# Performance work log

Hardware: AMD Instinct MI355X
Metric: run time of the kernel (lower is better)

Reference implementation:

```python
import jax, jax.numpy as jnp
import numpy as np

N_NODES = 100000
D = 128


def gcn_conv(x, W, b, src, dst, deg_inv_sqrt):
    # PyG GCNConv: linear transform, symmetric-normalized aggregation with self-loops, bias
    h = x @ W  # [N, D_out]
    norm = deg_inv_sqrt[src] * deg_inv_sqrt[dst]  # [E_tot]
    msgs = h[src] * norm[:, None]  # gather + scale  [E_tot, D_out]
    out = jax.ops.segment_sum(msgs, dst, num_segments=x.shape[0])  # scatter-add to targets
    return out + b


def _prep_edges(edge_index, n_nodes):
    # add self-loops (weight 1) and compute deg^{-1/2} over targets (flow source_to_target)
    loops = jnp.arange(n_nodes, dtype=edge_index.dtype)
    src = jnp.concatenate([edge_index[0], loops])
    dst = jnp.concatenate([edge_index[1], loops])
    deg = jax.ops.segment_sum(jnp.ones_like(dst, dtype=jnp.float32), dst, num_segments=n_nodes)
    deg_inv_sqrt = jnp.where(deg > 0, jax.lax.rsqrt(jnp.maximum(deg, 1.0)), 0.0)
    return src, dst, deg_inv_sqrt


def setup_inputs() -> dict:
    key = jax.random.key(0)
    ks = jax.random.split(key, 8)
    node_fts = jax.random.normal(ks[0], (N_NODES, D), dtype=jnp.float32)
    edge_index = jax.random.randint(ks[1], (2, 1600000), 0, N_NODES, dtype=jnp.int64)
    scale = 1.0 / np.sqrt(D)
    W1 = jax.random.uniform(ks[2], (D, D), jnp.float32, -scale, scale)
    b1 = jnp.zeros((D,), jnp.float32)
    W2 = jax.random.uniform(ks[3], (D, D), jnp.float32, -scale, scale)
    b2 = jnp.zeros((D,), jnp.float32)
    W3 = jax.random.uniform(ks[4], (D, D), jnp.float32, -scale, scale)
    b3 = jnp.zeros((D,), jnp.float32)
    return {"node_fts": node_fts, "edge_index": edge_index,
            "W1": W1, "b1": b1, "W2": W2, "b2": b2, "W3": W3, "b3": b3}


def reference(node_fts, edge_index, W1, b1, W2, b2, W3, b3):
    n = node_fts.shape[0]
    src, dst, dinv = _prep_edges(edge_index, n)
    x = jax.nn.relu(gcn_conv(node_fts, W1, b1, src, dst, dinv))
    x = jax.nn.relu(gcn_conv(x, W2, b2, src, dst, dinv))
    x = jax.nn.relu(gcn_conv(x, W3, b3, src, dst, dinv))
    return x
```

## Files before the change

kernel.cpp:

```cpp
#include <hip/hip_runtime.h>

#define NN 100000
#define EE 1600000
#define D 128
#define STRIDE 64
#define NPART 8
#define PSZ (NN / NPART)
#define NI4 (EE / 4)

typedef __attribute__((ext_vector_type(8))) short bf16x8;
typedef __attribute__((ext_vector_type(4))) float f32x4;

__device__ inline unsigned int f2bf2(float a, float b) {
    unsigned int ua = __float_as_uint(a);
    unsigned int ub = __float_as_uint(b);
    ua = (ua + 0x7fffu + ((ua >> 16) & 1u)) >> 16;
    ub = (ub + 0x7fffu + ((ub >> 16) & 1u)) >> 16;
    return ua | (ub << 16);
}
__device__ inline unsigned short f2bf(float a) {
    unsigned int u = __float_as_uint(a);
    return (unsigned short)((u + 0x7fffu + ((u >> 16) & 1u)) >> 16);
}
__device__ inline float2 bf2f2(unsigned int u) {
    return make_float2(__uint_as_float(u << 16), __uint_as_float(u & 0xffff0000u));
}


__global__ void init_kernel(int* __restrict__ cursor, unsigned int* __restrict__ hb) {
    int i = blockIdx.x * blockDim.x + threadIdx.x;
    if (i < NN) cursor[i] = 0;
    if (i < 64) hb[(size_t)NN * 64 + i] = 0;
}

__global__ __launch_bounds__(256) void scatter_part_kernel(const int4* __restrict__ src4,
                                                           const int4* __restrict__ dst4,
                                                           int* __restrict__ cursor,
                                                           int* __restrict__ csr) {
    const int p = blockIdx.x & (NPART - 1);
    const int bp = blockIdx.x >> 3;
    const int lo = p * PSZ, hi = lo + PSZ;
    for (int j = bp * 256 + threadIdx.x; j < NI4; j += 256 * 256) {
        int4 d4 = dst4[j];
        bool m0 = (d4.x >= lo && d4.x < hi);
        bool m1 = (d4.y >= lo && d4.y < hi);
        bool m2 = (d4.z >= lo && d4.z < hi);
        bool m3 = (d4.w >= lo && d4.w < hi);
        if (!(m0 | m1 | m2 | m3)) continue;
        int4 s4 = src4[j];
        if (m0) csr[d4.x * STRIDE + atomicAdd(&cursor[d4.x], 1)] = s4.x;
        if (m1) csr[d4.y * STRIDE + atomicAdd(&cursor[d4.y], 1)] = s4.y;
        if (m2) csr[d4.z * STRIDE + atomicAdd(&cursor[d4.z], 1)] = s4.z;
        if (m3) csr[d4.w * STRIDE + atomicAdd(&cursor[d4.w], 1)] = s4.w;
    }
}

__global__ void dinv_pad_kernel(const int* __restrict__ cursor, float* __restrict__ dinv,
                                int* __restrict__ csr) {
    int i = blockIdx.x * blockDim.x + threadIdx.x;
    if (i < NN) {
        int c = cursor[i];
        dinv[i] = rsqrtf(1.0f + (float)c);
        int e = i * STRIDE + c;
        const int end = i * STRIDE + ((c + 7) & ~7);
        for (; e < end; ++e) csr[e] = NN;
    }
}

__global__ void wt_build3_kernel(const float* __restrict__ W1, const float* __restrict__ W2,
                                 const float* __restrict__ W3, unsigned short* __restrict__ wt1,
                                 unsigned short* __restrict__ wt2, unsigned short* __restrict__ wt3) {
    const int which = blockIdx.x >> 6;
    const float* W = which == 0 ? W1 : (which == 1 ? W2 : W3);
    unsigned short* wt = which == 0 ? wt1 : (which == 1 ? wt2 : wt3);
    int i = (blockIdx.x & 63) * 256 + threadIdx.x;
    int n = i >> 7, k = i & 127;
    wt[n * 128 + k] = f2bf(W[k * 128 + n]);
}


template <bool F32IN>
__global__ __launch_bounds__(256) void gemm_mfma_kernel(const void* __restrict__ xin,
                                                        const unsigned short* __restrict__ wt,
                                                        const float* __restrict__ dinv,
                                                        unsigned int* __restrict__ hb) {
    const int wave = blockIdx.x * 4 + (threadIdx.x >> 6);
    const int m0 = wave * 16;
    if (m0 >= NN) return;
    const int lane = threadIdx.x & 63;
    const int r = lane & 15;
    const int q = lane >> 4;
    const unsigned short* wrow = wt + (size_t)r * 128 + q * 8;
    f32x4 acc[8] = {};
#pragma unroll
    for (int kc = 0; kc < 4; ++kc) {
        bf16x8 xf;
        if (F32IN) {
            const float* xrow = (const float*)xin + (size_t)(m0 + r) * 128 + q * 8 + kc * 32;
            float4 a = *(const float4*)xrow;
            float4 b = *(const float4*)(xrow + 4);
            unsigned short tmp[8] = {f2bf(a.x), f2bf(a.y), f2bf(a.z), f2bf(a.w),
                                     f2bf(b.x), f2bf(b.y), f2bf(b.z), f2bf(b.w)};
            xf = *(const bf16x8*)tmp;
        } else {
            const unsigned short* xrow =
                (const unsigned short*)xin + (size_t)(m0 + r) * 128 + q * 8 + kc * 32;
            xf = *(const bf16x8*)xrow;
        }
#pragma unroll
        for (int nt = 0; nt < 8; ++nt) {
            bf16x8 wf = *(const bf16x8*)(wrow + (size_t)nt * 16 * 128 + kc * 32);
            acc[nt] = __builtin_amdgcn_mfma_f32_16x16x32_bf16(wf, xf, acc[nt], 0, 0, 0);
        }
    }
    const float dvr = dinv[m0 + r];
    unsigned int* hrow = hb + (size_t)(m0 + r) * 64;
#pragma unroll
    for (int nt = 0; nt < 8; ++nt) {
        int n = nt * 16 + q * 4;
        *(uint2*)(hrow + (n >> 1)) =
            make_uint2(f2bf2(acc[nt][0] * dvr, acc[nt][1] * dvr),
                       f2bf2(acc[nt][2] * dvr, acc[nt][3] * dvr));
    }
}


template <bool BF16OUT>
__global__ __launch_bounds__(256) void aggregate_kernel(const unsigned int* __restrict__ hb,
                                                        const int* __restrict__ csr,
                                                        const int* __restrict__ cursor,
                                                        const float* __restrict__ dinv,
                                                        const float2* __restrict__ bias2,
                                                        void* __restrict__ outp) {
    const int d = blockIdx.x * 4 + (threadIdx.x >> 6);
    const int j = threadIdx.x & 63;
    const int nb = (cursor[d] + 7) >> 3;
    const int base = d * STRIDE;
    float2 acc = bf2f2(hb[(size_t)d * 64 + j]);
    for (int b = 0; b < nb; ++b) {
        const int e = base + b * 8;
        int4 c0 = *(const int4*)(csr + e);
        int4 c1 = *(const int4*)(csr + e + 4);
        unsigned int v0 = hb[(size_t)c0.x * 64 + j];
        unsigned int v1 = hb[(size_t)c0.y * 64 + j];
        unsigned int v2 = hb[(size_t)c0.z * 64 + j];
        unsigned int v3 = hb[(size_t)c0.w * 64 + j];
        unsigned int v4 = hb[(size_t)c1.x * 64 + j];
        unsigned int v5 = hb[(size_t)c1.y * 64 + j];
        unsigned int v6 = hb[(size_t)c1.z * 64 + j];
        unsigned int v7 = hb[(size_t)c1.w * 64 + j];
        float2 f0 = bf2f2(v0), f1 = bf2f2(v1), f2 = bf2f2(v2), f3 = bf2f2(v3);
        float2 f4 = bf2f2(v4), f5 = bf2f2(v5), f6 = bf2f2(v6), f7 = bf2f2(v7);
        acc.x += f0.x + f1.x + f2.x + f3.x + f4.x + f5.x + f6.x + f7.x;
        acc.y += f0.y + f1.y + f2.y + f3.y + f4.y + f5.y + f6.y + f7.y;
    }
    const float dv = dinv[d];
    float2 bb = bias2[j];
    float ox = fmaxf(dv * acc.x + bb.x, 0.0f);
    float oy = fmaxf(dv * acc.y + bb.y, 0.0f);
    if (BF16OUT) {
        ((unsigned int*)outp)[(size_t)d * 64 + j] = f2bf2(ox, oy);
    } else {
        ((float2*)outp)[(size_t)d * 64 + j] = make_float2(ox, oy);
    }
}


extern "C" void kernel_launch(void* const* d_in, const int* in_sizes, int n_in,
                              void* d_out, int out_size, void* d_ws, size_t ws_size,
                              hipStream_t stream) {
    const float* x0 = (const float*)d_in[0];
    const int* ei = (const int*)d_in[1];
    const float* W1 = (const float*)d_in[2];
    const float* b1 = (const float*)d_in[3];
    const float* W2 = (const float*)d_in[4];
    const float* b2 = (const float*)d_in[5];
    const float* W3 = (const float*)d_in[6];
    const float* b3 = (const float*)d_in[7];
    float* out = (float*)d_out;

    char* ws = (char*)d_ws;
    size_t off = 0;
    auto alloc = [&](size_t bytes) -> void* {
        off = (off + 511) & ~(size_t)511;
        void* p = ws + off;
        off += bytes;
        return p;
    };
    unsigned int* hb  = (unsigned int*)alloc(((size_t)NN + 1) * 64 * 4);
    int*   csr    = (int*)  alloc((size_t)NN * STRIDE * sizeof(int));
    int*   cursor = (int*)  alloc((size_t)NN * sizeof(int));
    float* dinv   = (float*)alloc((size_t)NN * sizeof(float));
    unsigned short* wt1 = (unsigned short*)alloc(128 * 128 * 2);
    unsigned short* wt2 = (unsigned short*)alloc(128 * 128 * 2);
    unsigned short* wt3 = (unsigned short*)alloc(128 * 128 * 2);

    unsigned int* xact = (unsigned int*)d_out;

    const int4* src4 = (const int4*)ei;
    const int4* dst4 = (const int4*)(ei + EE);

    init_kernel<<<(NN + 255) / 256, 256, 0, stream>>>(cursor, hb);
    scatter_part_kernel<<<2048, 256, 0, stream>>>(src4, dst4, cursor, csr);
    dinv_pad_kernel<<<(NN + 255) / 256, 256, 0, stream>>>(cursor, dinv, csr);
    wt_build3_kernel<<<192, 256, 0, stream>>>(W1, W2, W3, wt1, wt2, wt3);

    const int gemmBlocks = (NN / 16 + 3) / 4;

    gemm_mfma_kernel<true><<<gemmBlocks, 256, 0, stream>>>((const void*)x0, wt1, dinv, hb);
    aggregate_kernel<true><<<NN / 4, 256, 0, stream>>>(hb, csr, cursor, dinv,
                                                       (const float2*)b1, (void*)xact);
    gemm_mfma_kernel<false><<<gemmBlocks, 256, 0, stream>>>((const void*)xact, wt2, dinv, hb);
    aggregate_kernel<true><<<NN / 4, 256, 0, stream>>>(hb, csr, cursor, dinv,
                                                       (const float2*)b2, (void*)xact);
    gemm_mfma_kernel<false><<<gemmBlocks, 256, 0, stream>>>((const void*)xact, wt3, dinv, hb);
    aggregate_kernel<false><<<NN / 4, 256, 0, stream>>>(hb, csr, cursor, dinv,
                                                        (const float2*)b3, (void*)out);
}
```

Before: 475.6 us.

## Bin edges by destination partition before CSR scatter and unroll aggregation by 16

Adds a binning pass that groups edges into eight destination-range buckets through shared-memory staging, so the CSR scatter reads each partition's edges once instead of every partition block scanning the full edge list. The scatter then walks its bucket in two sub-ranges to keep cursor atomics localized. The aggregation loop now gathers 16 neighbors per iteration with a tree reduction, raising memory-level parallelism. The bucket capacity assumes roughly uniform destinations and adds an extra workspace buffer plus a kernel launch.

```diff
diff --git a/kernel.cpp b/kernel.cpp
--- a/kernel.cpp
+++ b/kernel.cpp
@@ -6,7 +6,8 @@
 #define STRIDE 64
 #define NPART 8
 #define PSZ (NN / NPART)
-#define NI4 (EE / 4)
+#define BCAP 204800
+#define BINCAP 512
 
 typedef __attribute__((ext_vector_type(8))) short bf16x8;
 typedef __attribute__((ext_vector_type(4))) float f32x4;
@@ -27,31 +28,68 @@
 }
 
 
-__global__ void init_kernel(int* __restrict__ cursor, unsigned int* __restrict__ hb) {
+__global__ void init_kernel(int* __restrict__ cursor, int* __restrict__ gcur,
+                            unsigned int* __restrict__ hb) {
     int i = blockIdx.x * blockDim.x + threadIdx.x;
     if (i < NN) cursor[i] = 0;
+    if (i < NPART) gcur[i] = 0;
     if (i < 64) hb[(size_t)NN * 64 + i] = 0;
 }
 
-__global__ __launch_bounds__(256) void scatter_part_kernel(const int4* __restrict__ src4,
-                                                           const int4* __restrict__ dst4,
-                                                           int* __restrict__ cursor,
-                                                           int* __restrict__ csr) {
+__global__ __launch_bounds__(256) void bin_kernel(const int* __restrict__ src,
+                                                  const int* __restrict__ dst,
+                                                  int* __restrict__ gcur,
+                                                  uint2* __restrict__ buckets) {
+    __shared__ uint2 bins[NPART][BINCAP];
+    __shared__ int bcnt[NPART];
+    __shared__ int gbase[NPART];
+    if (threadIdx.x < NPART) bcnt[threadIdx.x] = 0;
+    __syncthreads();
+    const int per = (EE + gridDim.x - 1) / gridDim.x;
+    const int lo = blockIdx.x * per;
+    const int hi = min(lo + per, EE);
+    for (int i = lo + threadIdx.x; i < hi; i += 256) {
+        int s = src[i], d = dst[i];
+        int b = d / PSZ;
+        int pos = atomicAdd(&bcnt[b], 1);
+        if (pos < BINCAP) {
+            bins[b][pos] = make_uint2((unsigned)s, (unsigned)d);
+        } else {
+            int gp = atomicAdd(&gcur[b], 1);
+            buckets[(size_t)b * BCAP + gp] = make_uint2((unsigned)s, (unsigned)d);
+        }
+    }
+    __syncthreads();
+    if (threadIdx.x < NPART) {
+        int c = min(bcnt[threadIdx.x], BINCAP);
+        gbase[threadIdx.x] = atomicAdd(&gcur[threadIdx.x], c);
+        bcnt[threadIdx.x] = c;
+    }
+    __syncthreads();
+    for (int b = 0; b < NPART; ++b) {
+        const int c = bcnt[b];
+        uint2* outp = buckets + (size_t)b * BCAP + gbase[b];
+        for (int i = threadIdx.x; i < c; i += 256) outp[i] = bins[b][i];
+    }
+}
+
+__global__ __launch_bounds__(256) void scatter2_kernel(const uint2* __restrict__ buckets,
+                                                       const int* __restrict__ gcur,
+                                                       int* __restrict__ cursor,
+                                                       int* __restrict__ csr) {
     const int p = blockIdx.x & (NPART - 1);
     const int bp = blockIdx.x >> 3;
-    const int lo = p * PSZ, hi = lo + PSZ;
-    for (int j = bp * 256 + threadIdx.x; j < NI4; j += 256 * 256) {
-        int4 d4 = dst4[j];
-        bool m0 = (d4.x >= lo && d4.x < hi);
-        bool m1 = (d4.y >= lo && d4.y < hi);
-        bool m2 = (d4.z >= lo && d4.z < hi);
-        bool m3 = (d4.w >= lo && d4.w < hi);
-        if (!(m0 | m1 | m2 | m3)) continue;
-        int4 s4 = src4[j];
-        if (m0) csr[d4.x * STRIDE + atomicAdd(&cursor[d4.x], 1)] = s4.x;
-        if (m1) csr[d4.y * STRIDE + atomicAdd(&cursor[d4.y], 1)] = s4.y;
-        if (m2) csr[d4.z * STRIDE + atomicAdd(&cursor[d4.z], 1)] = s4.z;
-        if (m3) csr[d4.w * STRIDE + atomicAdd(&cursor[d4.w], 1)] = s4.w;
+    const int cnt = gcur[p];
+    const uint2* bk = buckets + (size_t)p * BCAP;
+    const int mid = p * PSZ + PSZ / 2;
+#pragma unroll
+    for (int sub = 0; sub < 2; ++sub) {
+        for (int i = bp * 256 + threadIdx.x; i < cnt; i += 256 * 256) {
+            uint2 e = bk[i];
+            int d = (int)e.y;
+            bool in = (sub == 0) ? (d < mid) : (d >= mid);
+            if (in) csr[d * STRIDE + atomicAdd(&cursor[d], 1)] = (int)e.x;
+        }
     }
 }
 
@@ -134,11 +172,41 @@
                                                         void* __restrict__ outp) {
     const int d = blockIdx.x * 4 + (threadIdx.x >> 6);
     const int j = threadIdx.x & 63;
-    const int nb = (cursor[d] + 7) >> 3;
     const int base = d * STRIDE;
+    int e = base;
+    const int end = base + ((cursor[d] + 7) & ~7);
     float2 acc = bf2f2(hb[(size_t)d * 64 + j]);
-    for (int b = 0; b < nb; ++b) {
-        const int e = base + b * 8;
+    for (; e + 16 <= end; e += 16) {
+        int4 c0 = *(const int4*)(csr + e);
+        int4 c1 = *(const int4*)(csr + e + 4);
+        int4 c2 = *(const int4*)(csr + e + 8);
+        int4 c3 = *(const int4*)(csr + e + 12);
+        unsigned int v0 = hb[(size_t)c0.x * 64 + j];
+        unsigned int v1 = hb[(size_t)c0.y * 64 + j];
+        unsigned int v2 = hb[(size_t)c0.z * 64 + j];
+        unsigned int v3 = hb[(size_t)c0.w * 64 + j];
+        unsigned int v4 = hb[(size_t)c1.x * 64 + j];
+        unsigned int v5 = hb[(size_t)c1.y * 64 + j];
+        unsigned int v6 = hb[(size_t)c1.z * 64 + j];
+        unsigned int v7 = hb[(size_t)c1.w * 64 + j];
+        unsigned int v8 = hb[(size_t)c2.x * 64 + j];
+        unsigned int v9 = hb[(size_t)c2.y * 64 + j];
+        unsigned int va = hb[(size_t)c2.z * 64 + j];
+        unsigned int vb = hb[(size_t)c2.w * 64 + j];
+        unsigned int vc = hb[(size_t)c3.x * 64 + j];
+        unsigned int vd = hb[(size_t)c3.y * 64 + j];
+        unsigned int ve = hb[(size_t)c3.z * 64 + j];
+        unsigned int vf = hb[(size_t)c3.w * 64 + j];
+        float2 f0 = bf2f2(v0), f1 = bf2f2(v1), f2 = bf2f2(v2), f3 = bf2f2(v3);
+        float2 f4 = bf2f2(v4), f5 = bf2f2(v5), f6 = bf2f2(v6), f7 = bf2f2(v7);
+        float2 f8 = bf2f2(v8), f9 = bf2f2(v9), fa = bf2f2(va), fb = bf2f2(vb);
+        float2 fc = bf2f2(vc), fd = bf2f2(vd), fe = bf2f2(ve), ff = bf2f2(vf);
+        acc.x += ((f0.x + f1.x) + (f2.x + f3.x)) + ((f4.x + f5.x) + (f6.x + f7.x)) +
+                 ((f8.x + f9.x) + (fa.x + fb.x)) + ((fc.x + fd.x) + (fe.x + ff.x));
+        acc.y += ((f0.y + f1.y) + (f2.y + f3.y)) + ((f4.y + f5.y) + (f6.y + f7.y)) +
+                 ((f8.y + f9.y) + (fa.y + fb.y)) + ((fc.y + fd.y) + (fe.y + ff.y));
+    }
+    if (e < end) {
         int4 c0 = *(const int4*)(csr + e);
         int4 c1 = *(const int4*)(csr + e + 4);
         unsigned int v0 = hb[(size_t)c0.x * 64 + j];
@@ -151,8 +219,8 @@
         unsigned int v7 = hb[(size_t)c1.w * 64 + j];
         float2 f0 = bf2f2(v0), f1 = bf2f2(v1), f2 = bf2f2(v2), f3 = bf2f2(v3);
         float2 f4 = bf2f2(v4), f5 = bf2f2(v5), f6 = bf2f2(v6), f7 = bf2f2(v7);
-        acc.x += f0.x + f1.x + f2.x + f3.x + f4.x + f5.x + f6.x + f7.x;
-        acc.y += f0.y + f1.y + f2.y + f3.y + f4.y + f5.y + f6.y + f7.y;
+        acc.x += ((f0.x + f1.x) + (f2.x + f3.x)) + ((f4.x + f5.x) + (f6.x + f7.x));
+        acc.y += ((f0.y + f1.y) + (f2.y + f3.y)) + ((f4.y + f5.y) + (f6.y + f7.y));
     }
     const float dv = dinv[d];
     float2 bb = bias2[j];
@@ -189,19 +257,22 @@
     };
     unsigned int* hb  = (unsigned int*)alloc(((size_t)NN + 1) * 64 * 4);
     int*   csr    = (int*)  alloc((size_t)NN * STRIDE * sizeof(int));
+    uint2* buckets = (uint2*)alloc((size_t)NPART * BCAP * sizeof(uint2));
     int*   cursor = (int*)  alloc((size_t)NN * sizeof(int));
     float* dinv   = (float*)alloc((size_t)NN * sizeof(float));
+    int*   gcur   = (int*)  alloc(NPART * sizeof(int));
     unsigned short* wt1 = (unsigned short*)alloc(128 * 128 * 2);
     unsigned short* wt2 = (unsigned short*)alloc(128 * 128 * 2);
     unsigned short* wt3 = (unsigned short*)alloc(128 * 128 * 2);
 
     unsigned int* xact = (unsigned int*)d_out;
 
-    const int4* src4 = (const int4*)ei;
-    const int4* dst4 = (const int4*)(ei + EE);
-
-    init_kernel<<<(NN + 255) / 256, 256, 0, stream>>>(cursor, hb);
-    scatter_part_kernel<<<2048, 256, 0, stream>>>(src4, dst4, cursor, csr);
+    const int* src = ei;
+    const int* dst = ei + EE;
+
+    init_kernel<<<(NN + 255) / 256, 256, 0, stream>>>(cursor, gcur, hb);
+    bin_kernel<<<512, 256, 0, stream>>>(src, dst, gcur, buckets);
+    scatter2_kernel<<<2048, 256, 0, stream>>>(buckets, gcur, cursor, csr);
     dinv_pad_kernel<<<(NN + 255) / 256, 256, 0, stream>>>(cursor, dinv, csr);
     wt_build3_kernel<<<192, 256, 0, stream>>>(W1, W2, W3, wt1, wt2, wt3);
 
```

Result: slower. 488.1 us (+2.6%).

## Build compact CSR via two-pass shared-memory binning and block-local sort

Applied to the files above, without the earlier changes.

Replaces the per-node global-atomic scatter into a fixed-stride CSR with a two-stage build. The first pass bins edges by destination sub-block using shared-memory buckets with global overflow. The second pass sorts each sub-block locally in LDS to produce a compact padded CSR plus per-node offset/degree info and dinv. The aggregate kernel now reads offsets from info and processes 16 neighbors per iteration with a tree reduction. This aims to cut global atomic contention and scattered CSR writes, but relies on fixed capacities (SCAP, RCAP, LBCAP) that could overflow on skewed graphs.

```diff
diff --git a/kernel.cpp b/kernel.cpp
--- a/kernel.cpp
+++ b/kernel.cpp
@@ -3,10 +3,14 @@
 #define NN 100000
 #define EE 1600000
 #define D 128
-#define STRIDE 64
 #define NPART 8
 #define PSZ (NN / NPART)
 #define NI4 (EE / 4)
+#define SUBW 196
+#define NSB (NPART * 64)
+#define SCAP 4096
+#define RCAP 8192
+#define LBCAP 96
 
 typedef __attribute__((ext_vector_type(8))) short bf16x8;
 typedef __attribute__((ext_vector_type(4))) float f32x4;
@@ -27,43 +31,112 @@
 }
 
 
-__global__ void init_kernel(int* __restrict__ cursor, unsigned int* __restrict__ hb) {
+__global__ void init_kernel(int* __restrict__ gcur2, unsigned int* __restrict__ hb) {
     int i = blockIdx.x * blockDim.x + threadIdx.x;
-    if (i < NN) cursor[i] = 0;
+    if (i < NSB) gcur2[i] = 0;
     if (i < 64) hb[(size_t)NN * 64 + i] = 0;
 }
 
-__global__ __launch_bounds__(256) void scatter_part_kernel(const int4* __restrict__ src4,
-                                                           const int4* __restrict__ dst4,
-                                                           int* __restrict__ cursor,
-                                                           int* __restrict__ csr) {
-    const int p = blockIdx.x & (NPART - 1);
-    const int bp = blockIdx.x >> 3;
+__global__ __launch_bounds__(256) void filterbin_kernel(const int4* __restrict__ src4,
+                                                        const int4* __restrict__ dst4,
+                                                        int* __restrict__ gcur2,
+                                                        uint2* __restrict__ buckets2) {
+    __shared__ uint2 bins[64][LBCAP];
+    __shared__ int bcnt[64];
+    __shared__ int gbase[64];
+    const int p = blockIdx.x >> 6;
+    const int c = blockIdx.x & 63;
+    if (threadIdx.x < 64) bcnt[threadIdx.x] = 0;
+    __syncthreads();
     const int lo = p * PSZ, hi = lo + PSZ;
-    for (int j = bp * 256 + threadIdx.x; j < NI4; j += 256 * 256) {
-        int4 d4 = dst4[j];
+    const int chunk4 = NI4 / 64;
+    const int a0 = c * chunk4, a1 = a0 + chunk4;
+    for (int i = a0 + threadIdx.x; i < a1; i += 256) {
+        int4 d4 = dst4[i];
         bool m0 = (d4.x >= lo && d4.x < hi);
         bool m1 = (d4.y >= lo && d4.y < hi);
         bool m2 = (d4.z >= lo && d4.z < hi);
         bool m3 = (d4.w >= lo && d4.w < hi);
         if (!(m0 | m1 | m2 | m3)) continue;
-        int4 s4 = src4[j];
-        if (m0) csr[d4.x * STRIDE + atomicAdd(&cursor[d4.x], 1)] = s4.x;
-        if (m1) csr[d4.y * STRIDE + atomicAdd(&cursor[d4.y], 1)] = s4.y;
-        if (m2) csr[d4.z * STRIDE + atomicAdd(&cursor[d4.z], 1)] = s4.z;
-        if (m3) csr[d4.w * STRIDE + atomicAdd(&cursor[d4.w], 1)] = s4.w;
-    }
-}
-
-__global__ void dinv_pad_kernel(const int* __restrict__ cursor, float* __restrict__ dinv,
-                                int* __restrict__ csr) {
-    int i = blockIdx.x * blockDim.x + threadIdx.x;
-    if (i < NN) {
-        int c = cursor[i];
-        dinv[i] = rsqrtf(1.0f + (float)c);
-        int e = i * STRIDE + c;
-        const int end = i * STRIDE + ((c + 7) & ~7);
-        for (; e < end; ++e) csr[e] = NN;
+        int4 s4 = src4[i];
+        int ss[4] = {s4.x, s4.y, s4.z, s4.w};
+        int dd[4] = {d4.x, d4.y, d4.z, d4.w};
+        bool mm[4] = {m0, m1, m2, m3};
+#pragma unroll
+        for (int k = 0; k < 4; ++k) {
+            if (!mm[k]) continue;
+            int li = (dd[k] - lo) / SUBW;
+            int pos = atomicAdd(&bcnt[li], 1);
+            if (pos < LBCAP) {
+                bins[li][pos] = make_uint2((unsigned)ss[k], (unsigned)dd[k]);
+            } else {
+                int sb = p * 64 + li;
+                int gp = atomicAdd(&gcur2[sb], 1);
+                buckets2[(size_t)sb * SCAP + gp] = make_uint2((unsigned)ss[k], (unsigned)dd[k]);
+            }
+        }
+    }
+    __syncthreads();
+    if (threadIdx.x < 64) {
+        int cc = min(bcnt[threadIdx.x], LBCAP);
+        gbase[threadIdx.x] = atomicAdd(&gcur2[p * 64 + threadIdx.x], cc);
+        bcnt[threadIdx.x] = cc;
+    }
+    __syncthreads();
+    for (int b = 0; b < 64; ++b) {
+        const int cc = bcnt[b];
+        uint2* outp = buckets2 + (size_t)(p * 64 + b) * SCAP + gbase[b];
+        for (int i = threadIdx.x; i < cc; i += 256) outp[i] = bins[b][i];
+    }
+}
+
+__global__ __launch_bounds__(256) void sort3_kernel(const uint2* __restrict__ buckets2,
+                                                    const int* __restrict__ gcur2,
+                                                    int* __restrict__ csr,
+                                                    int* __restrict__ info,
+                                                    float* __restrict__ dinv) {
+    __shared__ int hist[256];
+    __shared__ int pscan[256];
+    __shared__ int lcur[256];
+    __shared__ int staged[RCAP];
+    const int sb = blockIdx.x;
+    const int li = sb & 63;
+    const int base_node = (sb >> 6) * PSZ + li * SUBW;
+    const int nnodes = min(SUBW, PSZ - li * SUBW);
+    const int scnt = gcur2[sb];
+    const uint2* bk = buckets2 + (size_t)sb * SCAP;
+    const int t = threadIdx.x;
+    hist[t] = 0;
+    __syncthreads();
+    for (int i = t; i < scnt; i += 256) atomicAdd(&hist[(int)bk[i].y - base_node], 1);
+    __syncthreads();
+    const int padded = (t < nnodes) ? ((hist[t] + 7) & ~7) : 0;
+    pscan[t] = padded;
+    __syncthreads();
+    for (int off = 1; off < 256; off <<= 1) {
+        int v = (t >= off) ? pscan[t - off] : 0;
+        __syncthreads();
+        pscan[t] += v;
+        __syncthreads();
+    }
+    const int rstart = pscan[t] - padded;
+    lcur[t] = rstart;
+    __syncthreads();
+    const int total = pscan[255];
+    for (int i = t; i < total; i += 256) staged[i] = NN;
+    __syncthreads();
+    for (int i = t; i < scnt; i += 256) {
+        uint2 r = bk[i];
+        int pos = atomicAdd(&lcur[(int)r.y - base_node], 1);
+        staged[pos] = (int)r.x;
+    }
+    __syncthreads();
+    int4* co = (int4*)(csr + (size_t)sb * RCAP);
+    for (int i = t; i < (total >> 2); i += 256) co[i] = ((const int4*)staged)[i];
+    if (t < nnodes) {
+        int dg = hist[t];
+        info[base_node + t] = ((sb * RCAP + rstart) << 8) | dg;
+        dinv[base_node + t] = rsqrtf(1.0f + (float)dg);
     }
 }
 
@@ -128,17 +201,47 @@
 template <bool BF16OUT>
 __global__ __launch_bounds__(256) void aggregate_kernel(const unsigned int* __restrict__ hb,
                                                         const int* __restrict__ csr,
-                                                        const int* __restrict__ cursor,
+                                                        const int* __restrict__ info,
                                                         const float* __restrict__ dinv,
                                                         const float2* __restrict__ bias2,
                                                         void* __restrict__ outp) {
     const int d = blockIdx.x * 4 + (threadIdx.x >> 6);
     const int j = threadIdx.x & 63;
-    const int nb = (cursor[d] + 7) >> 3;
-    const int base = d * STRIDE;
+    const int ifo = info[d];
+    int e = ifo >> 8;
+    const int end = e + (((ifo & 255) + 7) & ~7);
     float2 acc = bf2f2(hb[(size_t)d * 64 + j]);
-    for (int b = 0; b < nb; ++b) {
-        const int e = base + b * 8;
+    for (; e + 16 <= end; e += 16) {
+        int4 c0 = *(const int4*)(csr + e);
+        int4 c1 = *(const int4*)(csr + e + 4);
+        int4 c2 = *(const int4*)(csr + e + 8);
+        int4 c3 = *(const int4*)(csr + e + 12);
+        unsigned int v0 = hb[(size_t)c0.x * 64 + j];
+        unsigned int v1 = hb[(size_t)c0.y * 64 + j];
+        unsigned int v2 = hb[(size_t)c0.z * 64 + j];
+        unsigned int v3 = hb[(size_t)c0.w * 64 + j];
+        unsigned int v4 = hb[(size_t)c1.x * 64 + j];
+        unsigned int v5 = hb[(size_t)c1.y * 64 + j];
+        unsigned int v6 = hb[(size_t)c1.z * 64 + j];
+        unsigned int v7 = hb[(size_t)c1.w * 64 + j];
+        unsigned int v8 = hb[(size_t)c2.x * 64 + j];
+        unsigned int v9 = hb[(size_t)c2.y * 64 + j];
+        unsigned int va = hb[(size_t)c2.z * 64 + j];
+        unsigned int vb = hb[(size_t)c2.w * 64 + j];
+        unsigned int vc = hb[(size_t)c3.x * 64 + j];
+        unsigned int vd = hb[(size_t)c3.y * 64 + j];
+        unsigned int ve = hb[(size_t)c3.z * 64 + j];
+        unsigned int vf = hb[(size_t)c3.w * 64 + j];
+        float2 f0 = bf2f2(v0), f1 = bf2f2(v1), f2 = bf2f2(v2), f3 = bf2f2(v3);
+        float2 f4 = bf2f2(v4), f5 = bf2f2(v5), f6 = bf2f2(v6), f7 = bf2f2(v7);
+        float2 f8 = bf2f2(v8), f9 = bf2f2(v9), fa = bf2f2(va), fb = bf2f2(vb);
+        float2 fc = bf2f2(vc), fd = bf2f2(vd), fe = bf2f2(ve), ff = bf2f2(vf);
+        acc.x += ((f0.x + f1.x) + (f2.x + f3.x)) + ((f4.x + f5.x) + (f6.x + f7.x)) +
+                 ((f8.x + f9.x) + (fa.x + fb.x)) + ((fc.x + fd.x) + (fe.x + ff.x));
+        acc.y += ((f0.y + f1.y) + (f2.y + f3.y)) + ((f4.y + f5.y) + (f6.y + f7.y)) +
+                 ((f8.y + f9.y) + (fa.y + fb.y)) + ((fc.y + fd.y) + (fe.y + ff.y));
+    }
+    if (e < end) {
         int4 c0 = *(const int4*)(csr + e);
         int4 c1 = *(const int4*)(csr + e + 4);
         unsigned int v0 = hb[(size_t)c0.x * 64 + j];
@@ -151,8 +254,8 @@
         unsigned int v7 = hb[(size_t)c1.w * 64 + j];
         float2 f0 = bf2f2(v0), f1 = bf2f2(v1), f2 = bf2f2(v2), f3 = bf2f2(v3);
         float2 f4 = bf2f2(v4), f5 = bf2f2(v5), f6 = bf2f2(v6), f7 = bf2f2(v7);
-        acc.x += f0.x + f1.x + f2.x + f3.x + f4.x + f5.x + f6.x + f7.x;
-        acc.y += f0.y + f1.y + f2.y + f3.y + f4.y + f5.y + f6.y + f7.y;
+        acc.x += ((f0.x + f1.x) + (f2.x + f3.x)) + ((f4.x + f5.x) + (f6.x + f7.x));
+        acc.y += ((f0.y + f1.y) + (f2.y + f3.y)) + ((f4.y + f5.y) + (f6.y + f7.y));
     }
     const float dv = dinv[d];
     float2 bb = bias2[j];
@@ -188,9 +291,11 @@
         return p;
     };
     unsigned int* hb  = (unsigned int*)alloc(((size_t)NN + 1) * 64 * 4);
-    int*   csr    = (int*)  alloc((size_t)NN * STRIDE * sizeof(int));
-    int*   cursor = (int*)  alloc((size_t)NN * sizeof(int));
-    float* dinv   = (float*)alloc((size_t)NN * sizeof(float));
+    int*   csr     = (int*)  alloc((size_t)NSB * RCAP * sizeof(int));
+    uint2* buckets2 = (uint2*)alloc((size_t)NSB * SCAP * sizeof(uint2));
+    int*   info    = (int*)  alloc((size_t)NN * sizeof(int));
+    float* dinv    = (float*)alloc((size_t)NN * sizeof(float));
+    int*   gcur2   = (int*)  alloc(NSB * sizeof(int));
     unsigned short* wt1 = (unsigned short*)alloc(128 * 128 * 2);
     unsigned short* wt2 = (unsigned short*)alloc(128 * 128 * 2);
     unsigned short* wt3 = (unsigned short*)alloc(128 * 128 * 2);
@@ -200,20 +305,20 @@
     const int4* src4 = (const int4*)ei;
     const int4* dst4 = (const int4*)(ei + EE);
 
-    init_kernel<<<(NN + 255) / 256, 256, 0, stream>>>(cursor, hb);
-    scatter_part_kernel<<<2048, 256, 0, stream>>>(src4, dst4, cursor, csr);
-    dinv_pad_kernel<<<(NN + 255) / 256, 256, 0, stream>>>(cursor, dinv, csr);
+    init_kernel<<<2, 256, 0, stream>>>(gcur2, hb);
+    filterbin_kernel<<<NSB, 256, 0, stream>>>(src4, dst4, gcur2, buckets2);
+    sort3_kernel<<<NSB, 256, 0, stream>>>(buckets2, gcur2, csr, info, dinv);
     wt_build3_kernel<<<192, 256, 0, stream>>>(W1, W2, W3, wt1, wt2, wt3);
 
     const int gemmBlocks = (NN / 16 + 3) / 4;
 
     gemm_mfma_kernel<true><<<gemmBlocks, 256, 0, stream>>>((const void*)x0, wt1, dinv, hb);
-    aggregate_kernel<true><<<NN / 4, 256, 0, stream>>>(hb, csr, cursor, dinv,
+    aggregate_kernel<true><<<NN / 4, 256, 0, stream>>>(hb, csr, info, dinv,
                                                        (const float2*)b1, (void*)xact);
     gemm_mfma_kernel<false><<<gemmBlocks, 256, 0, stream>>>((const void*)xact, wt2, dinv, hb);
-    aggregate_kernel<true><<<NN / 4, 256, 0, stream>>>(hb, csr, cursor, dinv,
+    aggregate_kernel<true><<<NN / 4, 256, 0, stream>>>(hb, csr, info, dinv,
                                                        (const float2*)b2, (void*)xact);
     gemm_mfma_kernel<false><<<gemmBlocks, 256, 0, stream>>>((const void*)xact, wt3, dinv, hb);
-    aggregate_kernel<false><<<NN / 4, 256, 0, stream>>>(hb, csr, cursor, dinv,
+    aggregate_kernel<false><<<NN / 4, 256, 0, stream>>>(hb, csr, info, dinv,
                                                         (const float2*)b3, (void*)out);
 }
```

Result: faster. 434.7 us (-8.6%).
